# Performance work log

Hardware: AMD Instinct MI355X
Metric: run time of the kernel (lower is better)

Reference implementation:

```python
import jax, jax.numpy as jnp
import numpy as np

B, L1, L2, D = 128, 256, 256, 768
NEG = -10000.0
EPS = 1e-8


def setup_inputs() -> dict:
    key = jax.random.key(0)
    k1, k2, k3, k4 = jax.random.split(key, 4)
    v1 = jax.random.normal(k1, (B, L1, D), dtype=jnp.float32)
    v2 = jax.random.normal(k2, (B, L2, D), dtype=jnp.float32)
    # masks from random valid lengths in [L//2, L]
    len1 = jax.random.randint(k3, (B,), L1 // 2, L1 + 1)
    len2 = jax.random.randint(k4, (B,), L2 // 2, L2 + 1)
    mask1 = (jnp.arange(L1)[None, :] < len1[:, None]).astype(jnp.float32)
    mask2 = (jnp.arange(L2)[None, :] < len2[:, None]).astype(jnp.float32)
    return {"v1": v1, "mask1": mask1, "v2": v2, "mask2": mask2}


def reference(v1, mask1, v2, mask2):
    # alignment matrix [B, L1, L2]
    match = jnp.einsum('bld,bmd->blm', v1, v2)
    pair_mask = (mask1[:, :, None] * mask2[:, None, :]) > 0
    match = jnp.where(pair_mask, match, NEG)
    # attention over side 1: negative max-pool over L2, scaled
    s1 = -jnp.max(match, axis=2) / 100.0            # [B, L1]
    s1 = jnp.where(mask1 > 0, s1, NEG)
    attn1 = jax.nn.softmax(s1, axis=1)
    p1 = jnp.einsum('bld,bl->bd', v1, attn1)        # [B, D]
    # attention over side 2: negative max-pool over L1, scaled
    s2 = -jnp.max(match, axis=1) / 100.0            # [B, L2]
    s2 = jnp.where(mask2 > 0, s2, NEG)
    attn2 = jax.nn.softmax(s2, axis=1)
    p2 = jnp.einsum('bmd,bm->bd', v2, attn2)        # [B, D]
    # torch.nn.functional.cosine_similarity semantics (per-vector norm clamp)
    n1 = jnp.maximum(jnp.linalg.norm(p1, axis=-1), EPS)
    n2 = jnp.maximum(jnp.linalg.norm(p2, axis=-1), EPS)
    return jnp.sum(p1 * p2, axis=-1) / (n1 * n2)
```

## Files before the change

### kernel.cpp

```cpp
#include <hip/hip_runtime.h>


#define B_   128
#define L_   256
#define D_   768
#define NEGV (-10000.0f)

typedef _Float16 f16x8 __attribute__((ext_vector_type(8)));
typedef __fp16   h16x2 __attribute__((ext_vector_type(2)));
typedef float    f32x4 __attribute__((ext_vector_type(4)));

#define BT   128
#define BK   32
#define NKT  (D_ / BK)

__device__ __forceinline__ unsigned fmap(float f) {
    unsigned u = __float_as_uint(f);
    return (u & 0x80000000u) ? ~u : (u | 0x80000000u);
}
__device__ __forceinline__ float fdecode(unsigned u) {
    return __uint_as_float((u & 0x80000000u) ? (u ^ 0x80000000u) : ~u);
}
__device__ __forceinline__ float wred_max(float v) {
    #pragma unroll
    for (int o = 32; o; o >>= 1) v = fmaxf(v, __shfl_xor(v, o));
    return v;
}
__device__ __forceinline__ float wred_sum(float v) {
    #pragma unroll
    for (int o = 32; o; o >>= 1) v += __shfl_xor(v, o);
    return v;
}

__device__ __forceinline__ void gll16(const float* g, void* lds) {
    __builtin_amdgcn_global_load_lds(
        (const __attribute__((address_space(1))) void*)g,
        (__attribute__((address_space(3))) void*)lds, 16, 0, 0);
}

__device__ __forceinline__ f16x8 cvt8(float4 a, float4 b) {
    union { h16x2 h2[4]; f16x8 h8; } u;
    u.h2[0] = __builtin_amdgcn_cvt_pkrtz(a.x, a.y);
    u.h2[1] = __builtin_amdgcn_cvt_pkrtz(a.z, a.w);
    u.h2[2] = __builtin_amdgcn_cvt_pkrtz(b.x, b.y);
    u.h2[3] = __builtin_amdgcn_cvt_pkrtz(b.z, b.w);
    return u.h8;
}

__global__ __launch_bounds__(512, 4)
void k_match_max(const float* __restrict__ v1, const float* __restrict__ m1,
                 const float* __restrict__ v2, const float* __restrict__ m2,
                 unsigned* __restrict__ ru1, unsigned* __restrict__ ru2)
{
    __shared__ __align__(16) float As[2][BT * BK];
    __shared__ __align__(16) float Bs[2][BT * BK];
    __shared__ unsigned rU[BT], cU[BT];
    __shared__ float m1s[BT], m2s[BT];

    const int bid = blockIdx.x;
    const int wg  = (bid & 7) * 64 + (bid >> 3);
    const int b = wg >> 2, ti = (wg >> 1) & 1, tj = wg & 1;

    const int t = threadIdx.x;
    const int lane = t & 63, w = t >> 6;
    const int wr = w >> 1, wc = w & 1;
    const int fr = lane & 15, fg = lane >> 4;

    if (t < BT) {
        rU[t] = 0u; cU[t] = 0u;
        m1s[t] = m1[b * L_ + ti * BT + t];
        m2s[t] = m2[b * L_ + tj * BT + t];
    }

    const float* pa = v1 + ((size_t)b * L_ + ti * BT) * D_;
    const float* pb = v2 + ((size_t)b * L_ + tj * BT) * D_;

    const int r_in = lane >> 3;
    const int sblk = (lane & 7) ^ r_in;
    const int row0 = (w * 2 + 0) * 8 + r_in;
    const int row1 = (w * 2 + 1) * 8 + r_in;
    const float* ga0 = pa + (size_t)row0 * D_ + sblk * 4;
    const float* ga1 = pa + (size_t)row1 * D_ + sblk * 4;
    const float* gb0 = pb + (size_t)row0 * D_ + sblk * 4;
    const float* gb1 = pb + (size_t)row1 * D_ + sblk * 4;

    #define STAGE(buf, kt) do {                                   \
        int ko = (kt) * BK;                                       \
        gll16(ga0 + ko, &As[buf][(w * 2 + 0) * 256]);             \
        gll16(ga1 + ko, &As[buf][(w * 2 + 1) * 256]);             \
        gll16(gb0 + ko, &Bs[buf][(w * 2 + 0) * 256]);             \
        gll16(gb1 + ko, &Bs[buf][(w * 2 + 1) * 256]);             \
    } while (0)

    f32x4 acc[2][4] = {};
    STAGE(0, 0);
    __syncthreads();
    int cur = 0;
    for (int kt = 0; kt < NKT; ++kt) {
        if (kt + 1 < NKT) STAGE(cur ^ 1, kt + 1);
        f16x8 af[2], bf[4];
        #pragma unroll
        for (int i = 0; i < 2; ++i) {
            int r1 = wr * 32 + i * 16 + fr;
            const float* base = &As[cur][r1 * BK];
            float4 x = *(const float4*)(base + (((2 * fg + 0) ^ (fr & 7)) << 2));
            float4 y = *(const float4*)(base + (((2 * fg + 1) ^ (fr & 7)) << 2));
            af[i] = cvt8(x, y);
        }
        #pragma unroll
        for (int j = 0; j < 4; ++j) {
            int r2 = wc * 64 + j * 16 + fr;
            const float* base = &Bs[cur][r2 * BK];
            float4 x = *(const float4*)(base + (((2 * fg + 0) ^ (fr & 7)) << 2));
            float4 y = *(const float4*)(base + (((2 * fg + 1) ^ (fr & 7)) << 2));
            bf[j] = cvt8(x, y);
        }
        #pragma unroll
        for (int i = 0; i < 2; ++i)
            #pragma unroll
            for (int j = 0; j < 4; ++j)
                acc[i][j] = __builtin_amdgcn_mfma_f32_16x16x32_f16(af[i], bf[j], acc[i][j], 0, 0, 0);
        __syncthreads();
        cur ^= 1;
    }
    #undef STAGE

    #pragma unroll
    for (int i = 0; i < 2; ++i)
        #pragma unroll
        for (int r = 0; r < 4; ++r) {
            int row = wr * 32 + i * 16 + fg * 4 + r;
            bool rv = m1s[row] > 0.f;
            float mx = NEGV;
            #pragma unroll
            for (int j = 0; j < 4; ++j) {
                int col = wc * 64 + j * 16 + fr;
                float vv = (rv && m2s[col] > 0.f) ? acc[i][j][r] : NEGV;
                mx = fmaxf(mx, vv);
            }
            atomicMax(&rU[row], fmap(mx));
        }
    #pragma unroll
    for (int j = 0; j < 4; ++j) {
        int col = wc * 64 + j * 16 + fr;
        bool cv = m2s[col] > 0.f;
        float mx = NEGV;
        #pragma unroll
        for (int i = 0; i < 2; ++i)
            #pragma unroll
            for (int r = 0; r < 4; ++r) {
                int row = wr * 32 + i * 16 + fg * 4 + r;
                float vv = (cv && m1s[row] > 0.f) ? acc[i][j][r] : NEGV;
                mx = fmaxf(mx, vv);
            }
        atomicMax(&cU[col], fmap(mx));
    }
    __syncthreads();
    if (t < BT)            atomicMax(&ru1[b * L_ + ti * BT + t], rU[t]);
    else if (t < 2 * BT)   atomicMax(&ru2[b * L_ + tj * BT + (t - BT)], cU[t - BT]);
}

__global__ __launch_bounds__(256)
void k_attn_pool(const float* __restrict__ v1, const float* __restrict__ m1,
                 const float* __restrict__ v2, const float* __restrict__ m2,
                 const unsigned* __restrict__ ru1, const unsigned* __restrict__ ru2,
                 float* __restrict__ pout)
{
    const int lin = (int)blockIdx.x;
    const int swz = (lin & 7) * 96 + (lin >> 3);
    const int b = swz / 6, rem = swz % 6, side = rem / 3, chunk = rem % 3;

    const float* v     = side ? v2 : v1;
    const float* mk    = side ? m2 : m1;
    const unsigned* ru = side ? ru2 : ru1;
    const int t = threadIdx.x, lane = t & 63, w = t >> 6;

    __shared__ float attn[L_];
    __shared__ float sred[4];

    float mkv = mk[b * L_ + t];
    float s = (mkv > 0.f) ? (-fdecode(ru[b * L_ + t]) / 100.0f) : NEGV;

    float wm = wred_max(s);
    if (lane == 0) sred[w] = wm;
    __syncthreads();
    float mx = fmaxf(fmaxf(sred[0], sred[1]), fmaxf(sred[2], sred[3]));
    float e = expf(s - mx);
    __syncthreads();
    float ws = wred_sum(e);
    if (lane == 0) sred[w] = ws;
    __syncthreads();
    float sum = sred[0] + sred[1] + sred[2] + sred[3];
    attn[t] = e / sum;
    __syncthreads();

    const int d = chunk * 256 + t;
    const float* vb = v + (size_t)b * L_ * D_ + d;
    float p = 0.f;
    #pragma unroll 8
    for (int l = 0; l < L_; ++l) p += attn[l] * vb[(size_t)l * D_];
    pout[((size_t)b * 2 + side) * D_ + d] = p;
}

__global__ __launch_bounds__(256)
void k_cos(const float* __restrict__ pout, float* __restrict__ out)
{
    const int b = blockIdx.x, t = threadIdx.x, lane = t & 63, w = t >> 6;
    const float* p1 = pout + (size_t)b * 2 * D_;
    const float* p2 = p1 + D_;
    float dot = 0.f, n1 = 0.f, n2 = 0.f;
    for (int d = t; d < D_; d += 256) {
        float a = p1[d], c = p2[d];
        dot += a * c; n1 += a * a; n2 += c * c;
    }
    dot = wred_sum(dot); n1 = wred_sum(n1); n2 = wred_sum(n2);
    __shared__ float sd[4], sa[4], sc[4];
    if (lane == 0) { sd[w] = dot; sa[w] = n1; sc[w] = n2; }
    __syncthreads();
    if (t == 0) {
        float dd = sd[0] + sd[1] + sd[2] + sd[3];
        float aa = sa[0] + sa[1] + sa[2] + sa[3];
        float cc = sc[0] + sc[1] + sc[2] + sc[3];
        out[b] = dd / (fmaxf(sqrtf(aa), 1e-8f) * fmaxf(sqrtf(cc), 1e-8f));
    }
}

extern "C" void kernel_launch(void* const* d_in, const int* in_sizes, int n_in,
                              void* d_out, int out_size, void* d_ws, size_t ws_size,
                              hipStream_t stream)
{
    const float* v1 = (const float*)d_in[0];
    const float* m1 = (const float*)d_in[1];
    const float* v2 = (const float*)d_in[2];
    const float* m2 = (const float*)d_in[3];
    float* out = (float*)d_out;

    unsigned* ru1 = (unsigned*)d_ws;
    unsigned* ru2 = ru1 + (size_t)B_ * L_;
    float*    pout = (float*)(ru2 + (size_t)B_ * L_);

    (void)hipMemsetAsync(d_ws, 0, 2 * (size_t)B_ * L_ * sizeof(unsigned), stream);

    k_match_max<<<dim3((L_ / BT) * (L_ / BT) * B_), 512, 0, stream>>>(v1, m1, v2, m2, ru1, ru2);

    k_attn_pool<<<dim3(B_ * 2 * 3), 256, 0, stream>>>(v1, m1, v2, m2, ru1, ru2, pout);

    k_cos<<<B_, 256, 0, stream>>>(pout, out);
}
```

Measured before the change: 77.33 us.

## Stage GEMM tiles as fp16 in LDS via register prefetch with BK 64

```diff
diff --git a/kernel.cpp b/kernel.cpp
--- a/kernel.cpp
+++ b/kernel.cpp
@@ -11,8 +11,9 @@
 typedef float    f32x4 __attribute__((ext_vector_type(4)));
 
 #define BT   128
-#define BK   32
-#define NKT  (D_ / BK)
+#define BKF  64
+#define NKT  (D_ / BKF)
+#define LDH  72
 
 __device__ __forceinline__ unsigned fmap(float f) {
     unsigned u = __float_as_uint(f);
@@ -30,12 +31,6 @@
     #pragma unroll
     for (int o = 32; o; o >>= 1) v += __shfl_xor(v, o);
     return v;
-}
-
-__device__ __forceinline__ void gll16(const float* g, void* lds) {
-    __builtin_amdgcn_global_load_lds(
-        (const __attribute__((address_space(1))) void*)g,
-        (__attribute__((address_space(3))) void*)lds, 16, 0, 0);
 }
 
 __device__ __forceinline__ f16x8 cvt8(float4 a, float4 b) {
@@ -47,13 +42,13 @@
     return u.h8;
 }
 
-__global__ __launch_bounds__(512, 4)
+__global__ __launch_bounds__(512, 2)
 void k_match_max(const float* __restrict__ v1, const float* __restrict__ m1,
                  const float* __restrict__ v2, const float* __restrict__ m2,
                  unsigned* __restrict__ ru1, unsigned* __restrict__ ru2)
 {
-    __shared__ __align__(16) float As[2][BT * BK];
-    __shared__ __align__(16) float Bs[2][BT * BK];
+    __shared__ __align__(16) _Float16 As[2][BT * LDH];
+    __shared__ __align__(16) _Float16 Bs[2][BT * LDH];
     __shared__ unsigned rU[BT], cU[BT];
     __shared__ float m1s[BT], m2s[BT];
 
@@ -72,58 +67,65 @@
         m2s[t] = m2[b * L_ + tj * BT + t];
     }
 
-    const float* pa = v1 + ((size_t)b * L_ + ti * BT) * D_;
-    const float* pb = v2 + ((size_t)b * L_ + tj * BT) * D_;
-
-    const int r_in = lane >> 3;
-    const int sblk = (lane & 7) ^ r_in;
-    const int row0 = (w * 2 + 0) * 8 + r_in;
-    const int row1 = (w * 2 + 1) * 8 + r_in;
-    const float* ga0 = pa + (size_t)row0 * D_ + sblk * 4;
-    const float* ga1 = pa + (size_t)row1 * D_ + sblk * 4;
-    const float* gb0 = pb + (size_t)row0 * D_ + sblk * 4;
-    const float* gb1 = pb + (size_t)row1 * D_ + sblk * 4;
-
-    #define STAGE(buf, kt) do {                                   \
-        int ko = (kt) * BK;                                       \
-        gll16(ga0 + ko, &As[buf][(w * 2 + 0) * 256]);             \
-        gll16(ga1 + ko, &As[buf][(w * 2 + 1) * 256]);             \
-        gll16(gb0 + ko, &Bs[buf][(w * 2 + 0) * 256]);             \
-        gll16(gb1 + ko, &Bs[buf][(w * 2 + 1) * 256]);             \
+    const int grow = t >> 2;
+    const int c4   = t & 3;
+    const float* ga = v1 + ((size_t)b * L_ + ti * BT + grow) * D_ + c4 * 16;
+    const float* gb = v2 + ((size_t)b * L_ + tj * BT + grow) * D_ + c4 * 16;
+
+    float4 ra[4], rb[4];
+
+    #define GLOAD(kt) do {                                                    \
+        const float* A_ = ga + (kt) * BKF;                                    \
+        const float* C_ = gb + (kt) * BKF;                                    \
+        ra[0] = *(const float4*)(A_);      ra[1] = *(const float4*)(A_ + 4);  \
+        ra[2] = *(const float4*)(A_ + 8);  ra[3] = *(const float4*)(A_ + 12); \
+        rb[0] = *(const float4*)(C_);      rb[1] = *(const float4*)(C_ + 4);  \
+        rb[2] = *(const float4*)(C_ + 8);  rb[3] = *(const float4*)(C_ + 12); \
     } while (0)
 
+    #define DSWRITE(buf) do {                                                 \
+        _Float16* da = &As[buf][grow * LDH + c4 * 16];                        \
+        _Float16* db = &Bs[buf][grow * LDH + c4 * 16];                        \
+        *(f16x8*)da       = cvt8(ra[0], ra[1]);                               \
+        *(f16x8*)(da + 8) = cvt8(ra[2], ra[3]);                               \
+        *(f16x8*)db       = cvt8(rb[0], rb[1]);                               \
+        *(f16x8*)(db + 8) = cvt8(rb[2], rb[3]);                               \
+    } while (0)
+
     f32x4 acc[2][4] = {};
-    STAGE(0, 0);
+    GLOAD(0);
+    DSWRITE(0);
     __syncthreads();
     int cur = 0;
     for (int kt = 0; kt < NKT; ++kt) {
-        if (kt + 1 < NKT) STAGE(cur ^ 1, kt + 1);
-        f16x8 af[2], bf[4];
+        if (kt + 1 < NKT) GLOAD(kt + 1);
+        __builtin_amdgcn_sched_barrier(0);
         #pragma unroll
-        for (int i = 0; i < 2; ++i) {
-            int r1 = wr * 32 + i * 16 + fr;
-            const float* base = &As[cur][r1 * BK];
-            float4 x = *(const float4*)(base + (((2 * fg + 0) ^ (fr & 7)) << 2));
-            float4 y = *(const float4*)(base + (((2 * fg + 1) ^ (fr & 7)) << 2));
-            af[i] = cvt8(x, y);
+        for (int ks = 0; ks < 2; ++ks) {
+            f16x8 af[2], bf[4];
+            #pragma unroll
+            for (int i = 0; i < 2; ++i) {
+                int r1 = wr * 32 + i * 16 + fr;
+                af[i] = *(const f16x8*)&As[cur][r1 * LDH + ks * 32 + fg * 8];
+            }
+            #pragma unroll
+            for (int j = 0; j < 4; ++j) {
+                int r2 = wc * 64 + j * 16 + fr;
+                bf[j] = *(const f16x8*)&Bs[cur][r2 * LDH + ks * 32 + fg * 8];
+            }
+            #pragma unroll
+            for (int i = 0; i < 2; ++i)
+                #pragma unroll
+                for (int j = 0; j < 4; ++j)
+                    acc[i][j] = __builtin_amdgcn_mfma_f32_16x16x32_f16(af[i], bf[j], acc[i][j], 0, 0, 0);
         }
-        #pragma unroll
-        for (int j = 0; j < 4; ++j) {
-            int r2 = wc * 64 + j * 16 + fr;
-            const float* base = &Bs[cur][r2 * BK];
-            float4 x = *(const float4*)(base + (((2 * fg + 0) ^ (fr & 7)) << 2));
-            float4 y = *(const float4*)(base + (((2 * fg + 1) ^ (fr & 7)) << 2));
-            bf[j] = cvt8(x, y);
-        }
-        #pragma unroll
-        for (int i = 0; i < 2; ++i)
-            #pragma unroll
-            for (int j = 0; j < 4; ++j)
-                acc[i][j] = __builtin_amdgcn_mfma_f32_16x16x32_f16(af[i], bf[j], acc[i][j], 0, 0, 0);
+        __builtin_amdgcn_sched_barrier(0);
+        if (kt + 1 < NKT) DSWRITE(cur ^ 1);
         __syncthreads();
         cur ^= 1;
     }
-    #undef STAGE
+    #undef GLOAD
+    #undef DSWRITE
 
     #pragma unroll
     for (int i = 0; i < 2; ++i)
```

New measurement: 78.23 us. About the same (+1.2%).
